# Optimization experiments

Measured on AMD Instinct MI355X. Metric: run time of the kernel, lower is better.

The kernel has to match this reference:

```python
import jax, jax.numpy as jnp
import numpy as np
from jax import lax

V = 33          # n_vertices
B, H, W = 8, 1024, 1024
RES = 256       # backbone input resolution
N_FEATS = 128 * 8 * 8  # 8192


def setup_inputs() -> dict:
    key = jax.random.key(0)
    ks = jax.random.split(key, 16)
    inp = {"x": jax.random.uniform(ks[0], (B, 3, H, W), jnp.float32)}
    chans = [(3, 16), (16, 32), (32, 64), (64, 128), (128, 128)]
    for i, (ci, co) in enumerate(chans):
        inp[f"cw{i}"] = jax.random.normal(ks[1 + i], (co, ci, 3, 3), jnp.float32) / float(np.sqrt(ci * 9))
        inp[f"cb{i}"] = jnp.zeros((co,), jnp.float32)
    for i, c in enumerate([16, 32, 64, 128]):
        inp[f"g{i}"] = 1.0 + 0.02 * jax.random.normal(ks[6 + i], (c,), jnp.float32)  # InstanceNorm affine init
        inp[f"be{i}"] = jnp.zeros((c,), jnp.float32)
    inp["wg_w"] = 0.01 * jax.random.normal(ks[10], (3, N_FEATS), jnp.float32)
    inp["wg_b"] = jnp.ones((3,), jnp.float32)  # init_weights: ones bias
    # basis LUT bank: rank 0 = identity LUT (meshgrid, flip(0)), other ranks small noise
    grid = jnp.stack(jnp.meshgrid(*[jnp.arange(V, dtype=jnp.float32)] * 3, indexing="ij"), 0) / (V - 1)
    identity = jnp.flip(grid, 0).reshape(1, -1)          # [1, 3*V^3]
    rest = 0.01 * jax.random.normal(ks[11], (2, 3 * V ** 3), jnp.float32)
    inp["lut_w"] = jnp.concatenate([identity, rest], 0).T  # [3*V^3, n_ranks]
    inp["vertices"] = jnp.broadcast_to(jnp.arange(V, dtype=jnp.float32) / (V - 1), (3, V))[None]  # [1,3,V]
    return inp


def _conv(x, w, b, stride=2):
    y = lax.conv_general_dilated(x, w, (stride, stride), ((1, 1), (1, 1)),
                                 dimension_numbers=("NCHW", "OIHW", "NCHW"))
    return y + b[None, :, None, None]


def _inorm(x, g, be, eps=1e-5):
    m = x.mean((2, 3), keepdims=True)
    v = x.var((2, 3), keepdims=True)  # biased, matches torch InstanceNorm
    return (x - m) / jnp.sqrt(v + eps) * g[None, :, None, None] + be[None, :, None, None]


def _leaky(x):
    return jnp.where(x >= 0, x, 0.2 * x)


def _backbone(x, cws, cbs, gs, bes):
    h = jax.image.resize(x, (x.shape[0], 3, RES, RES), "bilinear")
    for i in range(4):  # Conv -> LeakyReLU -> InstanceNorm
        h = _inorm(_leaky(_conv(h, cws[i], cbs[i])), gs[i], bes[i])
    h = _leaky(_conv(h, cws[4], cbs[4]))  # last block, no norm; dropout = identity (eval)
    return h.reshape(x.shape[0], -1)


def _ailut(img, luts, vertices):
    # img [B,3,H,W], luts [B,3,V,V,V] (axes: out_ch, b, g, r), vertices [1,3,V]
    Bn, Vn = img.shape[0], vertices.shape[-1]
    verts = jnp.broadcast_to(vertices, (Bn, 3, Vn))
    q = img.reshape(Bn * 3, -1)
    vflat = verts.reshape(Bn * 3, Vn)
    idx = jax.vmap(lambda v, qq: jnp.searchsorted(v, qq, side="right"))(vflat, q) - 1
    idx = jnp.clip(idx, 0, Vn - 2).reshape(Bn, 3, -1)       # bin index per (b, color, pixel)
    lo = jnp.take_along_axis(verts, idx, axis=2)
    hi = jnp.take_along_axis(verts, idx + 1, axis=2)
    d = (img.reshape(Bn, 3, -1) - lo) / (hi - lo)           # fractional offset
    ir, ig, ib = idx[:, 0], idx[:, 1], idx[:, 2]
    dr, dg, db = d[:, 0], d[:, 1], d[:, 2]
    lflat = luts.reshape(Bn, 3, Vn ** 3)
    out = jnp.zeros_like(d)
    for ob in (0, 1):
        for og in (0, 1):
            for orr in (0, 1):
                w = ((db if ob else 1 - db) * (dg if og else 1 - dg) * (dr if orr else 1 - dr))
                lin = ((ib + ob) * Vn + (ig + og)) * Vn + (ir + orr)
                vals = jnp.take_along_axis(lflat, lin[:, None, :], axis=2)  # [B,3,N]
                out = out + w[:, None, :] * vals
    return out.reshape(img.shape)


def reference(x, cw0, cw1, cw2, cw3, cw4, cb0, cb1, cb2, cb3, cb4,
              g0, g1, g2, g3, be0, be1, be2, be3, wg_w, wg_b, lut_w, vertices):
    codes = _backbone(x, [cw0, cw1, cw2, cw3, cw4], [cb0, cb1, cb2, cb3, cb4],
                      [g0, g1, g2, g3], [be0, be1, be2, be3])   # [B, 8192]
    weights = codes @ wg_w.T + wg_b                              # [B, 3]
    luts = (weights @ lut_w.T).reshape(x.shape[0], 3, V, V, V)   # [B,3,V,V,V]
    outs = _ailut(x, luts, vertices)
    return outs, weights, luts, vertices
```

## Files before the change

### kernel.cpp

```cpp
#include <hip/hip_runtime.h>
#include <hip/hip_bf16.h>
#include <stdint.h>

typedef unsigned int U32;

static __device__ __forceinline__ U32 f2bf_rne(float f){
  U32 u; __builtin_memcpy(&u, &f, 4);
  u = (u + 0x7fffu + ((u >> 16) & 1u)) >> 16;
  return u & 0xffffu;
}
static __device__ __forceinline__ float bflo2f(U32 p){
  U32 u = p << 16; float f; __builtin_memcpy(&f, &u, 4); return f;
}
static __device__ __forceinline__ float bfhi2f(U32 p){
  U32 u = p & 0xffff0000u; float f; __builtin_memcpy(&f, &u, 4); return f;
}

__global__ void resize_k(const float* __restrict__ x, float* __restrict__ resz){
  __shared__ float hs[68][64];
  int blk = blockIdx.x;
  int tx = blk & 3;
  int ty = (blk >> 2) & 15;
  int bc = blk >> 6;
  int ox0 = tx << 6, oy0 = ty << 4;
  int r0 = 4*oy0 - 2; if (r0 < 0) r0 = 0;
  if (r0 > 956) r0 = 958;
  const float* src = x + ((size_t)bc << 20);
  #pragma unroll 4
  for (int i = threadIdx.x; i < 68*64; i += 256){
    int r   = i >> 6;
    int oxl = i & 63;
    int ox  = ox0 + oxl;
    int rr  = r0 + r; if (rr > 1023) rr = 1023;
    const float2* row2 = (const float2*)(src + ((size_t)rr << 10));
    float acc;
    if (ox >= 1 && ox <= 254){
      float2 a = row2[2*ox-1];
      float2 b = row2[2*ox];
      float2 c = row2[2*ox+1];
      float2 d = row2[2*ox+2];
      acc = (1.f/32)*(a.x + d.y)
          + (3.f/32)*(a.y + d.x)
          + (5.f/32)*(b.x + c.y)
          + (7.f/32)*(b.y + c.x);
    } else if (ox == 0){
      float2 a = row2[0], b = row2[1], c = row2[2];
      acc = (0.625f/3.5f)*a.x + (0.875f/3.5f)*a.y
          + (0.875f/3.5f)*b.x + (0.625f/3.5f)*b.y
          + (0.375f/3.5f)*c.x + (0.125f/3.5f)*c.y;
    } else {
      float2 a = row2[509], b = row2[510], c = row2[511];
      acc = (0.125f/3.5f)*a.x + (0.375f/3.5f)*a.y
          + (0.625f/3.5f)*b.x + (0.875f/3.5f)*b.y
          + (0.875f/3.5f)*c.x + (0.625f/3.5f)*c.y;
    }
    hs[r][oxl] = acc;
  }
  __syncthreads();
  for (int i = threadIdx.x; i < 16*64; i += 256){
    int oyl = i >> 6, oxl = i & 63;
    int oy = oy0 + oyl;
    float acc;
    if (oy >= 1 && oy <= 254){
      int j0 = 4*oy - 2 - r0;
      acc = (1.f/32)*(hs[j0+0][oxl] + hs[j0+7][oxl])
          + (3.f/32)*(hs[j0+1][oxl] + hs[j0+6][oxl])
          + (5.f/32)*(hs[j0+2][oxl] + hs[j0+5][oxl])
          + (7.f/32)*(hs[j0+3][oxl] + hs[j0+4][oxl]);
    } else if (oy == 0){
      acc = (0.625f/3.5f)*hs[0][oxl] + (0.875f/3.5f)*hs[1][oxl]
          + (0.875f/3.5f)*hs[2][oxl] + (0.625f/3.5f)*hs[3][oxl]
          + (0.375f/3.5f)*hs[4][oxl] + (0.125f/3.5f)*hs[5][oxl];
    } else {
      int j0 = 1018 - r0;
      acc = (0.125f/3.5f)*hs[j0+0][oxl] + (0.375f/3.5f)*hs[j0+1][oxl]
          + (0.625f/3.5f)*hs[j0+2][oxl] + (0.875f/3.5f)*hs[j0+3][oxl]
          + (0.875f/3.5f)*hs[j0+4][oxl] + (0.625f/3.5f)*hs[j0+5][oxl];
    }
    resz[((size_t)bc << 16) + ((size_t)oy << 8) + (size_t)(ox0 + oxl)] = acc;
  }
}

__global__ void conv0_k(const float* __restrict__ in, const float* __restrict__ w,
                        const float* __restrict__ bias, float* __restrict__ out,
                        float* __restrict__ st0){
  __shared__ float tile[3][5][264];
  __shared__ float wsm[432];
  __shared__ float bs[16];
  __shared__ float sred[4][16][2];
  int t = blockIdx.x & 63;
  int b = blockIdx.x >> 6;
  for (int i = threadIdx.x; i < 432; i += 256) wsm[i] = w[i];
  if (threadIdx.x < 16) bs[threadIdx.x] = bias[threadIdx.x];
  const float* inb = in + (size_t)b*3*65536;
  int ih0 = 4*t - 1;
  for (int i = threadIdx.x; i < 3*5*258; i += 256){
    int ci  = i / (5*258);
    int rem = i % (5*258);
    int r   = rem / 258;
    int cc  = rem % 258;
    int ih  = ih0 + r;
    int iw  = cc - 1;
    float v = 0.f;
    if ((unsigned)ih < 256u && (unsigned)iw < 256u)
      v = inb[ci*65536 + ih*256 + iw];
    tile[ci][r][cc] = v;
  }
  __syncthreads();
  int lr = threadIdx.x >> 7;
  int ow = threadIdx.x & 127;
  float acc[16];
  #pragma unroll
  for (int j = 0; j < 16; j++) acc[j] = 0.f;
  #pragma unroll
  for (int ci = 0; ci < 3; ci++)
    #pragma unroll
    for (int kh = 0; kh < 3; kh++)
      #pragma unroll
      for (int kw = 0; kw < 3; kw++){
        float v = tile[ci][2*lr + kh][2*ow + kw];
        #pragma unroll
        for (int j = 0; j < 16; j++)
          acc[j] += v * wsm[j*27 + ci*9 + kh*3 + kw];
      }
  int s = t*256 + (int)threadIdx.x;
  size_t obase = (size_t)b*16*16384 + (size_t)s;
  float av[16];
  #pragma unroll
  for (int j = 0; j < 16; j++){
    float a = acc[j] + bs[j];
    a = (a >= 0.f) ? a : 0.2f*a;
    av[j] = a;
    out[obase + (size_t)j*16384] = a;
  }
  int wv = threadIdx.x >> 6;
  #pragma unroll
  for (int j = 0; j < 16; j++){
    float s1 = av[j], s2 = av[j]*av[j];
    #pragma unroll
    for (int o = 32; o > 0; o >>= 1){ s1 += __shfl_down(s1, o, 64); s2 += __shfl_down(s2, o, 64); }
    if ((threadIdx.x & 63) == 0){ sred[wv][j][0] = s1; sred[wv][j][1] = s2; }
  }
  __syncthreads();
  if (threadIdx.x < 16){
    float s1 = 0.f, s2 = 0.f;
    #pragma unroll
    for (int w2 = 0; w2 < 4; w2++){ s1 += sred[w2][threadIdx.x][0]; s2 += sred[w2][threadIdx.x][1]; }
    float* e = st0 + (((size_t)b*16 + threadIdx.x)*64 + t)*2;
    e[0] = s1; e[1] = s2;
  }
}

template<int CI, int CO, int IN, int OUT, int COB, int SPLIT, int TIN, int TOUT>
__global__ void __launch_bounds__(256, 1)
conv_leaky_k(const float* __restrict__ in, const float* __restrict__ w,
             const float* __restrict__ bias, float* __restrict__ out,
             const float* __restrict__ st_in, const float* __restrict__ g,
             const float* __restrict__ be, float* __restrict__ st_out){
  constexpr int P     = 256 / SPLIT;
  constexpr int TILES = (OUT*OUT + P - 1) / P;
  constexpr int CIS   = CI / SPLIT;
  constexpr int SUBS  = (TIN > 0) ? ((256/CI < TIN) ? 256/CI : TIN) : 1;
  int blk  = blockIdx.x;
  int b    = blk & 7;
  int rest = blk >> 3;
  int tile = rest % TILES;
  int cob  = rest / TILES;
  int co0  = cob * COB;
  __shared__ float ws[COB * CI * 9];
  __shared__ float bs[COB];
  __shared__ float red[(SPLIT > 1) ? 256 * COB : 1];
  __shared__ float sc[(TIN > 0) ? CI : 1];
  __shared__ float sh[(TIN > 0) ? CI : 1];
  __shared__ float pre[(TIN > 0) ? CI : 1][SUBS][2];
  for (int i = threadIdx.x; i < COB*CI*9; i += 256) ws[i] = w[(size_t)co0*CI*9 + i];
  if (threadIdx.x < COB) bs[threadIdx.x] = bias[co0 + threadIdx.x];
  if constexpr (TIN > 0){
    int c = threadIdx.x / SUBS, sub = threadIdx.x % SUBS;
    if (c < CI){
      const float* e = st_in + ((size_t)b*CI + c)*TIN*2;
      float s1 = 0.f, s2 = 0.f;
      for (int t2 = sub; t2 < TIN; t2 += SUBS){ s1 += e[t2*2]; s2 += e[t2*2+1]; }
      pre[c][sub][0] = s1; pre[c][sub][1] = s2;
    }
  }
  __syncthreads();
  if constexpr (TIN > 0){
    if (threadIdx.x < CI){
      float s1 = 0.f, s2 = 0.f;
      #pragma unroll
      for (int t2 = 0; t2 < SUBS; t2++){ s1 += pre[threadIdx.x][t2][0]; s2 += pre[threadIdx.x][t2][1]; }
      constexpr float hw = (float)(IN*IN);
      float mean = s1 * (1.f/hw);
      float var  = s2 * (1.f/hw) - mean*mean;
      float rstd = 1.f / sqrtf(var + 1e-5f);
      float scv  = g[threadIdx.x] * rstd;
      sc[threadIdx.x] = scv;
      sh[threadIdx.x] = be[threadIdx.x] - mean*scv;
    }
  }
  __syncthreads();
  int pix = threadIdx.x % P;
  int sp  = threadIdx.x / P;
  int s   = tile*P + pix;
  int oh = s / OUT, ow = s % OUT;
  float acc[COB];
  #pragma unroll
  for (int j = 0; j < COB; j++) acc[j] = 0.f;
  const float* inb = in + ((size_t)b*CI + sp*CIS) * (IN*IN);
  #pragma unroll
  for (int c0 = 0; c0 < CIS; c0 += 4){
    constexpr int CH = (CIS < 4) ? CIS : 4;
    #pragma unroll
    for (int kh = 0; kh < 3; kh++){
      int ih = oh*2 - 1 + kh;
      if ((unsigned)ih >= (unsigned)IN) continue;
      #pragma unroll
      for (int kw = 0; kw < 3; kw++){
        int iw = ow*2 - 1 + kw;
        if ((unsigned)iw >= (unsigned)IN) continue;
        const float* p0 = inb + (size_t)c0*(IN*IN) + ih*IN + iw;
        float vv[CH];
        #pragma unroll
        for (int ci = 0; ci < CH; ci++) vv[ci] = p0[(size_t)ci*(IN*IN)];
        if constexpr (TIN > 0){
          #pragma unroll
          for (int ci = 0; ci < CH; ci++) vv[ci] = vv[ci]*sc[sp*CIS+c0+ci] + sh[sp*CIS+c0+ci];
        }
        #pragma unroll
        for (int ci = 0; ci < CH; ci++){
          #pragma unroll
          for (int j = 0; j < COB; j++)
            acc[j] += vv[ci] * ws[j*CI*9 + (sp*CIS+c0+ci)*9 + kh*3 + kw];
        }
      }
    }
  }
  if constexpr (SPLIT > 1){
    #pragma unroll
    for (int j = 0; j < COB; j++) red[threadIdx.x*COB + j] = acc[j];
    __syncthreads();
    if (sp == 0){
      #pragma unroll
      for (int s2 = 1; s2 < SPLIT; s2++)
        #pragma unroll
        for (int j = 0; j < COB; j++)
          acc[j] += red[(pix + s2*P)*COB + j];
    }
  }
  float av[COB];
  if (sp == 0){
    size_t obase = ((size_t)b*CO + co0) * (size_t)(OUT*OUT) + s;
    #pragma unroll
    for (int j = 0; j < COB; j++){
      float a = acc[j] + bs[j];
      a = (a >= 0.f) ? a : 0.2f*a;
      av[j] = a;
      out[obase + (size_t)j*OUT*OUT] = a;
    }
  }
  if constexpr (TOUT > 0){
    constexpr int NW = P / 64;
    __shared__ float sred2[NW][COB][2];
    if (threadIdx.x < P){
      #pragma unroll
      for (int j = 0; j < COB; j++){
        float s1 = av[j], s2 = av[j]*av[j];
        #pragma unroll
        for (int o = 32; o > 0; o >>= 1){ s1 += __shfl_down(s1, o, 64); s2 += __shfl_down(s2, o, 64); }
        if ((threadIdx.x & 63) == 0){ int wv = threadIdx.x >> 6; sred2[wv][j][0] = s1; sred2[wv][j][1] = s2; }
      }
    }
    __syncthreads();
    if (threadIdx.x < COB){
      float s1 = 0.f, s2 = 0.f;
      #pragma unroll
      for (int wv = 0; wv < NW; wv++){ s1 += sred2[wv][threadIdx.x][0]; s2 += sred2[wv][threadIdx.x][1]; }
      float* e = st_out + (((size_t)b*CO + co0 + threadIdx.x)*TOUT + tile)*2;
      e[0] = s1; e[1] = s2;
    }
  }
}

__global__ void __launch_bounds__(256, 1)
conv4_gemv_k(const float* __restrict__ in, const float* __restrict__ w,
             const float* __restrict__ bias, const float* __restrict__ st_in,
             const float* __restrict__ g, const float* __restrict__ be,
             const float* __restrict__ wgw, float* __restrict__ part){
  __shared__ float ws[4*128*9];
  __shared__ float bs[4];
  __shared__ float red[256*4];
  __shared__ float sc[128], sh[128];
  __shared__ float pre[128][2][2];
  int blk = blockIdx.x;
  int b   = blk & 7;
  int cob = blk >> 3;
  int co0 = cob * 4;
  for (int i = threadIdx.x; i < 4*128*9; i += 256) ws[i] = w[(size_t)co0*128*9 + i];
  if (threadIdx.x < 4) bs[threadIdx.x] = bias[co0 + threadIdx.x];
  {
    int c = threadIdx.x >> 1, sub = threadIdx.x & 1;
    if (c < 128){
      const float* e = st_in + ((size_t)b*128 + c)*2*2;
      pre[c][sub][0] = e[sub*2]; pre[c][sub][1] = e[sub*2+1];
    }
  }
  __syncthreads();
  if (threadIdx.x < 128){
    float s1 = pre[threadIdx.x][0][0] + pre[threadIdx.x][1][0];
    float s2 = pre[threadIdx.x][0][1] + pre[threadIdx.x][1][1];
    float mean = s1 * (1.f/256.f);
    float var  = s2 * (1.f/256.f) - mean*mean;
    float rstd = 1.f / sqrtf(var + 1e-5f);
    float scv  = g[threadIdx.x] * rstd;
    sc[threadIdx.x] = scv;
    sh[threadIdx.x] = be[threadIdx.x] - mean*scv;
  }
  __syncthreads();
  int pix = threadIdx.x & 63;
  int sp  = threadIdx.x >> 6;
  int s   = pix;
  int oh = s >> 3, ow = s & 7;
  float acc[4];
  #pragma unroll
  for (int j = 0; j < 4; j++) acc[j] = 0.f;
  const float* inb = in + ((size_t)b*128 + sp*32) * 256;
  #pragma unroll
  for (int c0 = 0; c0 < 32; c0 += 4){
    #pragma unroll
    for (int kh = 0; kh < 3; kh++){
      int ih = oh*2 - 1 + kh;
      if ((unsigned)ih >= 16u) continue;
      #pragma unroll
      for (int kw = 0; kw < 3; kw++){
        int iw = ow*2 - 1 + kw;
        if ((unsigned)iw >= 16u) continue;
        const float* p0 = inb + (size_t)c0*256 + ih*16 + iw;
        float vv[4];
        #pragma unroll
        for (int ci = 0; ci < 4; ci++) vv[ci] = p0[ci*256];
        #pragma unroll
        for (int ci = 0; ci < 4; ci++) vv[ci] = vv[ci]*sc[sp*32+c0+ci] + sh[sp*32+c0+ci];
        #pragma unroll
        for (int ci = 0; ci < 4; ci++){
          #pragma unroll
          for (int j = 0; j < 4; j++)
            acc[j] += vv[ci] * ws[j*128*9 + (sp*32+c0+ci)*9 + kh*3 + kw];
        }
      }
    }
  }
  #pragma unroll
  for (int j = 0; j < 4; j++) red[threadIdx.x*4 + j] = acc[j];
  __syncthreads();
  if (sp == 0){
    #pragma unroll
    for (int s2 = 1; s2 < 4; s2++)
      #pragma unroll
      for (int j = 0; j < 4; j++)
        acc[j] += red[(pix + s2*64)*4 + j];
    float av[4];
    #pragma unroll
    for (int j = 0; j < 4; j++){
      float a = acc[j] + bs[j];
      av[j] = (a >= 0.f) ? a : 0.2f*a;
    }
    float p3[3];
    #pragma unroll
    for (int o = 0; o < 3; o++){
      float t = 0.f;
      #pragma unroll
      for (int j = 0; j < 4; j++)
        t += av[j] * wgw[(size_t)o*8192 + (size_t)(co0+j)*64 + s];
      #pragma unroll
      for (int off = 32; off > 0; off >>= 1) t += __shfl_down(t, off, 64);
      p3[o] = t;
    }
    if (pix == 0){
      float* e = part + ((size_t)b*32 + cob)*3;
      e[0] = p3[0]; e[1] = p3[1]; e[2] = p3[2];
    }
  }
}

__global__ void luts_k(const float* __restrict__ part, const float* __restrict__ wgb,
                       const float* __restrict__ lut_w, const float* __restrict__ verts,
                       U32* __restrict__ lp, float* __restrict__ outp){
  __shared__ float wf_s[24];
  if (threadIdx.x < 24){
    int b = threadIdx.x / 3, o = threadIdx.x % 3;
    float s = 0.f;
    for (int cob = 0; cob < 32; cob++) s += part[((size_t)b*32 + cob)*3 + o];
    s += wgb[o];
    wf_s[threadIdx.x] = s;
    if (blockIdx.x == 0) outp[25165824 + threadIdx.x] = s;
  }
  __syncthreads();
  if (blockIdx.x == 0 && threadIdx.x < 99) outp[26028336 + threadIdx.x] = verts[threadIdx.x];
  int j = blockIdx.x * 256 + threadIdx.x;
  if (j >= 107811) return;
  int jn = (j + 1 < 107811) ? (j + 1) : j;
  float l0 = lut_w[3*j+0], l1 = lut_w[3*j+1], l2 = lut_w[3*j+2];
  float m0 = lut_w[3*jn+0], m1 = lut_w[3*jn+1], m2 = lut_w[3*jn+2];
  int c = j / 35937;
  int i = j - c * 35937;
  #pragma unroll
  for (int b = 0; b < 8; b++){
    float w0 = wf_s[b*3+0], w1 = wf_s[b*3+1], w2 = wf_s[b*3+2];
    float v  = w0*l0 + w1*l1 + w2*l2;
    float vn = w0*m0 + w1*m1 + w2*m2;
    outp[25165848 + (size_t)b*107811 + j] = v;
    lp[(size_t)(b*3 + c)*35940 + i] = f2bf_rne(v) | (f2bf_rne(vn) << 16);
  }
}

static __device__ __forceinline__ void apply_phase(const U32* ls, const float4* rv,
                                                   const float4* gv, const float4* bv,
                                                   float* ob, int base){
  #pragma unroll
  for (int k = 0; k < 4; k++){
    float rr[4] = {rv[k].x, rv[k].y, rv[k].z, rv[k].w};
    float gg[4] = {gv[k].x, gv[k].y, gv[k].z, gv[k].w};
    float bb[4] = {bv[k].x, bv[k].y, bv[k].z, bv[k].w};
    U32 pw[4][4];
    float w00[4], w01[4], w10[4], w11[4], drx[4];
    #pragma unroll
    for (int h = 0; h < 4; h++){
      float rq = rr[h] * 32.f;
      float gq = gg[h] * 32.f;
      float bq = bb[h] * 32.f;
      int ir = (int)rq; ir = ir > 31 ? 31 : ir;
      int ig = (int)gq; ig = ig > 31 ? 31 : ig;
      int ib = (int)bq; ib = ib > 31 ? 31 : ib;
      float dr = rq - (float)ir;
      float dg = gq - (float)ig;
      float db = bq - (float)ib;
      int lin = (ib*33 + ig)*33 + ir;
      pw[h][0] = ls[lin];
      pw[h][1] = ls[lin+33];
      pw[h][2] = ls[lin+1089];
      pw[h][3] = ls[lin+1122];
      float t = db*dg;
      w11[h] = t;
      w10[h] = db - t;
      w01[h] = dg - t;
      w00[h] = 1.f - db - dg + t;
      drx[h] = dr;
    }
    float res[4];
    #pragma unroll
    for (int h = 0; h < 4; h++){
      float odr = 1.f - drx[h];
      float v0 = odr*bflo2f(pw[h][0]) + drx[h]*bfhi2f(pw[h][0]);
      float v1 = odr*bflo2f(pw[h][1]) + drx[h]*bfhi2f(pw[h][1]);
      float v2 = odr*bflo2f(pw[h][2]) + drx[h]*bfhi2f(pw[h][2]);
      float v3 = odr*bflo2f(pw[h][3]) + drx[h]*bfhi2f(pw[h][3]);
      res[h] = w00[h]*v0 + w01[h]*v1 + w10[h]*v2 + w11[h]*v3;
    }
    *(float4*)(ob + base + k*4096) = make_float4(res[0], res[1], res[2], res[3]);
  }
}

__global__ void __launch_bounds__(1024, 4) ailut_apply_k(const float* __restrict__ x,
                                                         const U32* __restrict__ lp,
                                                         float* __restrict__ outp){
  __shared__ U32 ls[35936];
  int b = blockIdx.z, c = blockIdx.y;
  const size_t plane = 1048576;
  const float* xb = x + (size_t)b*3*plane;
  int base = blockIdx.x * 32768 + (int)threadIdx.x*4;
  float4 rv[4], gv[4], bv[4];
  #pragma unroll
  for (int k = 0; k < 4; k++){
    int p0 = base + k*4096;
    rv[k] = *(const float4*)(xb + p0);
    gv[k] = *(const float4*)(xb + plane + p0);
    bv[k] = *(const float4*)(xb + 2*plane + p0);
  }
  const U32* lsrc = lp + (size_t)(b*3 + c)*35940;
  for (int i = threadIdx.x; i < 8984; i += 1024)
    __builtin_amdgcn_global_load_lds(
        (const __attribute__((address_space(1))) void*)(lsrc + 4*(size_t)i),
        (__attribute__((address_space(3))) void*)(ls + 4*i), 16, 0, 0);
  __syncthreads();
  float* ob = outp + ((size_t)b*3 + c)*plane;
  apply_phase(ls, rv, gv, bv, ob, base);
  #pragma unroll
  for (int k = 0; k < 4; k++){
    int p0 = base + 16384 + k*4096;
    rv[k] = *(const float4*)(xb + p0);
    gv[k] = *(const float4*)(xb + plane + p0);
    bv[k] = *(const float4*)(xb + 2*plane + p0);
  }
  apply_phase(ls, rv, gv, bv, ob, base + 16384);
}

extern "C" void kernel_launch(void* const* d_in, const int* in_sizes, int n_in,
                              void* d_out, int out_size, void* d_ws, size_t ws_size,
                              hipStream_t stream){
  const float* x    = (const float*)d_in[0];
  const float* cw0  = (const float*)d_in[1];
  const float* cb0  = (const float*)d_in[2];
  const float* cw1  = (const float*)d_in[3];
  const float* cb1  = (const float*)d_in[4];
  const float* cw2  = (const float*)d_in[5];
  const float* cb2  = (const float*)d_in[6];
  const float* cw3  = (const float*)d_in[7];
  const float* cb3  = (const float*)d_in[8];
  const float* cw4  = (const float*)d_in[9];
  const float* cb4  = (const float*)d_in[10];
  const float* g0   = (const float*)d_in[11];
  const float* be0  = (const float*)d_in[12];
  const float* g1   = (const float*)d_in[13];
  const float* be1  = (const float*)d_in[14];
  const float* g2   = (const float*)d_in[15];
  const float* be2  = (const float*)d_in[16];
  const float* g3   = (const float*)d_in[17];
  const float* be3  = (const float*)d_in[18];
  const float* wgw  = (const float*)d_in[19];
  const float* wgb  = (const float*)d_in[20];
  const float* lutw = (const float*)d_in[21];
  const float* vert = (const float*)d_in[22];
  float* out = (float*)d_out;
  float* ws  = (float*)d_ws;

  U32*   lp   = (U32*)ws;
  float* st0  = ws + 862720;
  float* st1  = ws + 879104;
  float* st2  = ws + 887296;
  float* st3  = ws + 891392;
  float* resz = ws + 895488;
  float* act0 = ws + 2468352;
  float* act1 = act0 + 2097152;
  float* act2 = act1 + 1048576;
  float* act3 = act2 + 524288;
  float* part = act3 + 262144;

  resize_k<<<1536, 256, 0, stream>>>(x, resz);

  conv0_k<<<512, 256, 0, stream>>>(resz, cw0, cb0, act0, st0);
  conv_leaky_k<16,32,128,64,8,1,64,16>
      <<<8*4*16, 256, 0, stream>>>(act0, cw1, cb1, act1, st0, g0, be0, st1);
  conv_leaky_k<32,64,64,32,4,1,16,4>
      <<<8*16*4, 256, 0, stream>>>(act1, cw2, cb2, act2, st1, g1, be1, st2);
  conv_leaky_k<64,128,32,16,4,2,4,2>
      <<<8*32*2, 256, 0, stream>>>(act2, cw3, cb3, act3, st2, g2, be2, st3);
  conv4_gemv_k<<<256, 256, 0, stream>>>(act3, cw4, cb4, st3, g3, be3, wgw, part);

  luts_k<<<422, 256, 0, stream>>>(part, wgb, lutw, vert, lp, out);
  ailut_apply_k<<<dim3(32,3,8), 1024, 0, stream>>>(x, lp, out);
}
```

Before: 182.6 us.

## Store LUT as packed bf16 singles to halve LDS footprint in apply kernel

The per-channel LUT in shared memory changes from pre-paired 32-bit entries (value plus r-neighbour) to single 16-bit bf16 values, with neighbour pairs rebuilt at runtime from two 32-bit LDS reads and a shift. This halves LDS use per block (about 72KB down to about 36KB) and the global-to-LDS copy volume, and launch bounds are raised to allow more resident blocks. The cost is up to twice as many LDS reads per trilinear lookup plus extra ALU for the unaligned pair assembly.

```diff
diff --git a/kernel.cpp b/kernel.cpp
--- a/kernel.cpp
+++ b/kernel.cpp
@@ -3,6 +3,7 @@
 #include <stdint.h>
 
 typedef unsigned int U32;
+typedef unsigned short U16;
 
 static __device__ __forceinline__ U32 f2bf_rne(float f){
   U32 u; __builtin_memcpy(&u, &f, 4);
@@ -385,7 +386,7 @@
 
 __global__ void luts_k(const float* __restrict__ part, const float* __restrict__ wgb,
                        const float* __restrict__ lut_w, const float* __restrict__ verts,
-                       U32* __restrict__ lp, float* __restrict__ outp){
+                       U16* __restrict__ lp16, float* __restrict__ outp){
   __shared__ float wf_s[24];
   if (threadIdx.x < 24){
     int b = threadIdx.x / 3, o = threadIdx.x % 3;
@@ -399,22 +400,25 @@
   if (blockIdx.x == 0 && threadIdx.x < 99) outp[26028336 + threadIdx.x] = verts[threadIdx.x];
   int j = blockIdx.x * 256 + threadIdx.x;
   if (j >= 107811) return;
-  int jn = (j + 1 < 107811) ? (j + 1) : j;
   float l0 = lut_w[3*j+0], l1 = lut_w[3*j+1], l2 = lut_w[3*j+2];
-  float m0 = lut_w[3*jn+0], m1 = lut_w[3*jn+1], m2 = lut_w[3*jn+2];
   int c = j / 35937;
   int i = j - c * 35937;
   #pragma unroll
   for (int b = 0; b < 8; b++){
     float w0 = wf_s[b*3+0], w1 = wf_s[b*3+1], w2 = wf_s[b*3+2];
     float v  = w0*l0 + w1*l1 + w2*l2;
-    float vn = w0*m0 + w1*m1 + w2*m2;
     outp[25165848 + (size_t)b*107811 + j] = v;
-    lp[(size_t)(b*3 + c)*35940 + i] = f2bf_rne(v) | (f2bf_rne(vn) << 16);
-  }
-}
-
-static __device__ __forceinline__ void apply_phase(const U32* ls, const float4* rv,
+    lp16[(size_t)(b*3 + c)*35940 + i] = (U16)f2bf_rne(v);
+  }
+}
+
+static __device__ __forceinline__ U32 mkpair(const U32* W, int s){
+  U32 A = W[s >> 1];
+  U32 B = W[(s + 1) >> 1];
+  return (s & 1) ? ((A >> 16) | (B << 16)) : A;
+}
+
+static __device__ __forceinline__ void apply_phase(const U32* W, const float4* rv,
                                                    const float4* gv, const float4* bv,
                                                    float* ob, int base){
   #pragma unroll
@@ -436,10 +440,10 @@
       float dg = gq - (float)ig;
       float db = bq - (float)ib;
       int lin = (ib*33 + ig)*33 + ir;
-      pw[h][0] = ls[lin];
-      pw[h][1] = ls[lin+33];
-      pw[h][2] = ls[lin+1089];
-      pw[h][3] = ls[lin+1122];
+      pw[h][0] = mkpair(W, lin);
+      pw[h][1] = mkpair(W, lin + 33);
+      pw[h][2] = mkpair(W, lin + 1089);
+      pw[h][3] = mkpair(W, lin + 1122);
       float t = db*dg;
       w11[h] = t;
       w10[h] = db - t;
@@ -461,10 +465,10 @@
   }
 }
 
-__global__ void __launch_bounds__(1024, 4) ailut_apply_k(const float* __restrict__ x,
-                                                         const U32* __restrict__ lp,
+__global__ void __launch_bounds__(1024, 8) ailut_apply_k(const float* __restrict__ x,
+                                                         const U16* __restrict__ lp16,
                                                          float* __restrict__ outp){
-  __shared__ U32 ls[35936];
+  __shared__ U16 ls16[35952];
   int b = blockIdx.z, c = blockIdx.y;
   const size_t plane = 1048576;
   const float* xb = x + (size_t)b*3*plane;
@@ -477,14 +481,15 @@
     gv[k] = *(const float4*)(xb + plane + p0);
     bv[k] = *(const float4*)(xb + 2*plane + p0);
   }
-  const U32* lsrc = lp + (size_t)(b*3 + c)*35940;
-  for (int i = threadIdx.x; i < 8984; i += 1024)
+  const U16* lsrc = lp16 + (size_t)(b*3 + c)*35940;
+  for (int i = threadIdx.x; i < 4493; i += 1024)
     __builtin_amdgcn_global_load_lds(
-        (const __attribute__((address_space(1))) void*)(lsrc + 4*(size_t)i),
-        (__attribute__((address_space(3))) void*)(ls + 4*i), 16, 0, 0);
-  __syncthreads();
+        (const __attribute__((address_space(1))) void*)(lsrc + 8*(size_t)i),
+        (__attribute__((address_space(3))) void*)(ls16 + 8*i), 16, 0, 0);
+  __syncthreads();
+  const U32* W = (const U32*)ls16;
   float* ob = outp + ((size_t)b*3 + c)*plane;
-  apply_phase(ls, rv, gv, bv, ob, base);
+  apply_phase(W, rv, gv, bv, ob, base);
   #pragma unroll
   for (int k = 0; k < 4; k++){
     int p0 = base + 16384 + k*4096;
@@ -492,7 +497,7 @@
     gv[k] = *(const float4*)(xb + plane + p0);
     bv[k] = *(const float4*)(xb + 2*plane + p0);
   }
-  apply_phase(ls, rv, gv, bv, ob, base + 16384);
+  apply_phase(W, rv, gv, bv, ob, base + 16384);
 }
 
 extern "C" void kernel_launch(void* const* d_in, const int* in_sizes, int n_in,
@@ -524,7 +529,7 @@
   float* out = (float*)d_out;
   float* ws  = (float*)d_ws;
 
-  U32*   lp   = (U32*)ws;
+  U16*   lp16 = (U16*)ws;
   float* st0  = ws + 862720;
   float* st1  = ws + 879104;
   float* st2  = ws + 887296;
@@ -547,6 +552,6 @@
       <<<8*32*2, 256, 0, stream>>>(act2, cw3, cb3, act3, st2, g2, be2, st3);
   conv4_gemv_k<<<256, 256, 0, stream>>>(act3, cw4, cb4, st3, g3, be3, wgw, part);
 
-  luts_k<<<422, 256, 0, stream>>>(part, wgb, lutw, vert, lp, out);
-  ailut_apply_k<<<dim3(32,3,8), 1024, 0, stream>>>(x, lp, out);
-}
+  luts_k<<<422, 256, 0, stream>>>(part, wgb, lutw, vert, lp16, out);
+  ailut_apply_k<<<dim3(32,3,8), 1024, 0, stream>>>(x, lp16, out);
+}
```

After: 218.9 us. 19.9% more time.
